# Performance work log

Hardware: AMD Instinct MI355X
Metric: run time of the kernel (lower is better)

## Reference

```python
import jax, jax.numpy as jnp
import numpy as np

N_STEPS = 8          # spatial_interval
SPATIAL_SCALE = 1.0  # spatial_scale


def setup_inputs() -> dict:
    key = jax.random.key(0)
    ks = jax.random.split(key, 6)
    B, N, D = 32, 1024, 256
    x = jax.random.normal(ks[0], (B, N, D), dtype=jnp.float32)
    adj_mx = jax.random.uniform(ks[1], (N, N), dtype=jnp.float32) / N  # row-scaled dense adjacency
    alpha_train = jnp.ones((N,), dtype=jnp.float32)          # alpha * ones(num_node), alpha=1.0
    w = jnp.eye(D, dtype=jnp.float32) + 0.01 * jax.random.normal(ks[2], (D, D), dtype=jnp.float32)
    d = jax.random.uniform(ks[3], (D,), dtype=jnp.float32)
    fc_in_w = jax.random.normal(ks[4], (D, D), dtype=jnp.float32) * (1.0 / np.sqrt(D))
    fc_in_b = jnp.zeros((D,), dtype=jnp.float32)
    return {"x": x, "adj_mx": adj_mx, "alpha_train": alpha_train, "w": w,
            "d": d, "fc_in_w": fc_in_w, "fc_in_b": fc_in_b, "vt": 0}


def reference(x, adj_mx, alpha_train, w, d, fc_in_w, fc_in_b, vt):
    # x: [B, N, D]. x0 is detached in torch (x.clone().detach()).
    x0 = jax.lax.stop_gradient(x)
    # fc_in (dropout is identity in eval mode)
    h = jnp.einsum('bnd,ed->bne', x, fc_in_w) + fc_in_b
    # constants of the diffusion ODE
    alph = jax.nn.sigmoid(alpha_train)[:, None]          # [N, 1]
    d_clamped = jnp.clip(d, 0.0, 1.0)
    w_eff = (w * d_clamped) @ w.T                        # [D, D]
    dt = jnp.float32(SPATIAL_SCALE / N_STEPS)

    def euler_step(h, _):
        ax = jnp.einsum('nm,bmd->bnd', adj_mx, h)        # graph diffusion
        f = alph * 0.5 * (ax - h) + h @ w_eff - h + x0
        return h + dt * f, None

    h, _ = jax.lax.scan(euler_step, h, None, length=N_STEPS)
    return h
```

## Files before the change

kernel.cpp:

```cpp
#include <hip/hip_runtime.h>
#include <hip/hip_bf16.h>
#include <stdint.h>

typedef __bf16 bf16;
typedef __bf16 bf16x8 __attribute__((ext_vector_type(8)));
typedef __bf16 bf16x4 __attribute__((ext_vector_type(4)));
typedef float f32x4 __attribute__((ext_vector_type(4)));
typedef unsigned short u16;

__device__ __forceinline__ void gload_lds16(const bf16* g, bf16* l) {
    __builtin_amdgcn_global_load_lds(
        (const __attribute__((address_space(1))) void*)g,
        (__attribute__((address_space(3))) void*)l, 16, 0, 0);
}

__device__ __forceinline__ void stChunk(const bf16* __restrict__ g, int ld,
                                        bf16* l, int c) {
    int row = c >> 3, slot = c & 7;
    gload_lds16(g + (size_t)row * ld + ((slot ^ (row & 7)) << 3), l + c * 8);
}

#define LDSW(buf, row, kc) \
    (*(const bf16x8*)&(buf)[(row) * 64 + ((((kc) ^ ((row) & 7))) << 3)])

__global__ void prep_alpha(const float* __restrict__ a, float* __restrict__ out) {
    int i = blockIdx.x * blockDim.x + threadIdx.x;
    if (i < 1024) out[i] = 0.5f / (1.0f + __expf(-a[i]));
}

__global__ void prep_adj(const float* __restrict__ adj, const float* __restrict__ ahs,
                         bf16* __restrict__ adjb) {
    int i = blockIdx.x * blockDim.x + threadIdx.x;
    int row = i >> 8;
    float s = ahs[row];
    float4 v = ((const float4*)adj)[i];
    bf16x4 o = {(bf16)(s * v.x), (bf16)(s * v.y), (bf16)(s * v.z), (bf16)(s * v.w)};
    ((bf16x4*)adjb)[i] = o;
}

__global__ void cast_f32_bf16x4(const float* __restrict__ src, bf16* __restrict__ dst,
                                int n4) {
    int i = blockIdx.x * blockDim.x + threadIdx.x;
    if (i < n4) {
        float4 v = ((const float4*)src)[i];
        bf16x4 o = {(bf16)v.x, (bf16)v.y, (bf16)v.z, (bf16)v.w};
        ((bf16x4*)dst)[i] = o;
    }
}

__global__ void prep_weff(const float* __restrict__ w, const float* __restrict__ dv,
                          bf16* __restrict__ weffT) {
    __shared__ float wk[256];
    __shared__ float dd[256];
    int k = blockIdx.x, j = threadIdx.x;
    dd[j] = fminf(fmaxf(dv[j], 0.0f), 1.0f);
    wk[j] = w[k * 256 + j];
    __syncthreads();
    float s = 0.0f;
#pragma unroll 8
    for (int c = 0; c < 256; ++c) s += wk[c] * dd[c] * w[j * 256 + c];
    weffT[j * 256 + k] = (bf16)s;
}

__global__ void prep_xT(const float* __restrict__ x, bf16* __restrict__ xT,
                        bf16* __restrict__ xb) {
    __shared__ bf16 tile[64][65];
    int b = blockIdx.z, n0 = blockIdx.x * 64, d0 = blockIdx.y * 64;
    int t = threadIdx.x;
    int i = t >> 4, j4 = (t & 15) * 4;
#pragma unroll
    for (int p = 0; p < 4; ++p) {
        int n = i + p * 16;
        size_t gi = (((size_t)b << 10) + n0 + n) * 256 + d0 + j4;
        float4 v = *(const float4*)&x[gi];
        bf16x4 o = {(bf16)v.x, (bf16)v.y, (bf16)v.z, (bf16)v.w};
        *(bf16x4*)&xb[gi] = o;
        tile[n][j4 + 0] = o[0]; tile[n][j4 + 1] = o[1];
        tile[n][j4 + 2] = o[2]; tile[n][j4 + 3] = o[3];
    }
    __syncthreads();
#pragma unroll
    for (int p = 0; p < 4; ++p) {
        int c = p * 256 + t;
        int d = c >> 4, nc = c & 15;
        bf16x4 o = {tile[nc * 4 + 0][d], tile[nc * 4 + 1][d],
                    tile[nc * 4 + 2][d], tile[nc * 4 + 3][d]};
        *(bf16x4*)&xT[(((size_t)(b * 256 + d0 + d)) << 10) + n0 + nc * 4] = o;
    }
}

__device__ __forceinline__ void stageA4(const bf16* __restrict__ g, int lda,
                                        bf16* l, int t) {
#pragma unroll
    for (int i = 0; i < 4; ++i) stChunk(g, lda, l, (i << 8) + t);
}
__device__ __forceinline__ void stageB2(const bf16* __restrict__ g, int ldb,
                                        bf16* l, int t) {
#pragma unroll
    for (int i = 0; i < 2; ++i) stChunk(g, ldb, l, (i << 8) + t);
}

__device__ __forceinline__ void mma_tile(const bf16* A, const bf16* B,
                                         f32x4 acc[2][4], int lane, int wv) {
    const int r0 = wv * 32 + (lane & 15);
    const int kq = lane >> 4;
    bf16x8 a[2][2], b[4][2];
#pragma unroll
    for (int mi = 0; mi < 2; ++mi) {
        int rA = r0 + mi * 16;
#pragma unroll
        for (int kk = 0; kk < 2; ++kk) a[mi][kk] = LDSW(A, rA, kk * 4 + kq);
    }
#pragma unroll
    for (int ni = 0; ni < 4; ++ni) {
        int rB = ni * 16 + (lane & 15);
#pragma unroll
        for (int kk = 0; kk < 2; ++kk) b[ni][kk] = LDSW(B, rB, kk * 4 + kq);
    }
#pragma unroll
    for (int kk = 0; kk < 2; ++kk)
#pragma unroll
        for (int mi = 0; mi < 2; ++mi)
#pragma unroll
            for (int ni = 0; ni < 4; ++ni)
                acc[mi][ni] = __builtin_amdgcn_mfma_f32_16x16x32_bf16(
                    a[mi][kk], b[ni][kk], acc[mi][ni], 0, 0, 0);
}

template <int NT, typename F>
__device__ __forceinline__ void run_pipeline(F tadr, bf16 (*As)[8192],
                                             bf16 (*Bs)[4096], f32x4 acc[2][4],
                                             int t, int lane, int wv) {
    {
        const bf16 *Ag, *Bg; int lda, ldb;
        tadr(0, Ag, lda, Bg, ldb);
        stageA4(Ag, lda, As[0], t);
        stageB2(Bg, ldb, Bs[0], t);
        if (NT > 1) {
            tadr(1, Ag, lda, Bg, ldb);
            stageA4(Ag, lda, As[1], t);
            stageB2(Bg, ldb, Bs[1], t);
        }
    }
    int cur = 0, pre = 2;
#pragma unroll 1
    for (int i = 0; i < NT; ++i) {
        if (i + 2 < NT) {
            const bf16 *Ag, *Bg; int lda, ldb;
            tadr(i + 2, Ag, lda, Bg, ldb);
            stageA4(Ag, lda, As[pre], t);
            stageB2(Bg, ldb, Bs[pre], t);
            asm volatile("s_waitcnt vmcnt(12)" ::: "memory");
        } else if (i + 1 < NT) {
            asm volatile("s_waitcnt vmcnt(6)" ::: "memory");
        } else {
            asm volatile("s_waitcnt vmcnt(0)" ::: "memory");
        }
        __builtin_amdgcn_s_barrier();
        __builtin_amdgcn_s_setprio(1);
        mma_tile(As[cur], Bs[cur], acc, lane, wv);
        __builtin_amdgcn_s_setprio(0);
        __builtin_amdgcn_s_barrier();
        cur = (cur == 2) ? 0 : cur + 1;
        pre = (pre == 2) ? 0 : pre + 1;
    }
}

__launch_bounds__(256, 2)
__global__ void gemm_fcin(const bf16* __restrict__ xb, const bf16* __restrict__ fcwb,
                          const float* __restrict__ fcb,
                          bf16* __restrict__ hb, bf16* __restrict__ hT,
                          bf16* __restrict__ hloT) {
    __shared__ __align__(16) bf16 As[3][8192];
    __shared__ __align__(16) bf16 Bs[3][4096];
    int t = threadIdx.x, lane = t & 63, wv = t >> 6;
    int row0 = blockIdx.y * 128;
    int col0 = blockIdx.x * 64;
    f32x4 acc[2][4] = {};
    const bf16* Ab = xb + (size_t)row0 * 256;
    const bf16* Bb = fcwb + (size_t)col0 * 256;
    auto tadr = [&](int i, const bf16*& Ag, int& lda, const bf16*& Bg, int& ldb) {
        Ag = Ab + i * 64; lda = 256;
        Bg = Bb + i * 64; ldb = 256;
    };
    run_pipeline<4>(tadr, As, Bs, acc, t, lane, wv);

    int rbase = row0 + wv * 32 + ((lane >> 4) << 2);
    int cbase = col0 + (lane & 15);
#pragma unroll
    for (int mi = 0; mi < 2; ++mi) {
        int rg = rbase + mi * 16;
#pragma unroll
        for (int ni = 0; ni < 4; ++ni) {
            int col = cbase + ni * 16;
            float bias = fcb[col];
            bf16x4 tv, lv;
#pragma unroll
            for (int r = 0; r < 4; ++r) {
                float v = acc[mi][ni][r] + bias;
                size_t idx = (size_t)(rg + r) * 256 + col;
                bf16 hi = (bf16)v;
                hb[idx] = hi;
                tv[r] = hi;
                lv[r] = (bf16)(v - (float)hi);
            }
            int b = rg >> 10, n = rg & 1023;
            size_t tb = (((size_t)(b * 256 + col)) << 10) + n;
            *(bf16x4*)&hT[tb] = tv;
            *(bf16x4*)&hloT[tb] = lv;
        }
    }
}

template <bool LAST>
__launch_bounds__(512, 1)
__global__ void gemm_step(const bf16* __restrict__ adjb, const bf16* __restrict__ hbp,
                          const bf16* __restrict__ hTp, const bf16* __restrict__ weffT,
                          const float* __restrict__ ahs, const bf16* __restrict__ xT,
                          bf16* __restrict__ hloT, bf16* __restrict__ hbn,
                          bf16* __restrict__ hTn, float* __restrict__ out) {
    __shared__ __align__(16) char smem[147456];
    bf16 (*As)[16384] = (bf16(*)[16384])smem;
    bf16 (*Bs)[8192]  = (bf16(*)[8192])(smem + 98304);
    int t = threadIdx.x, lane = t & 63, wv = t >> 6;
    int wm = wv >> 1, wn = wv & 1;
    int g = blockIdx.x;
    int xcd = g & 7, bidx = g >> 3;
    int b = (bidx & 3) * 8 + xcd;
    int tile = bidx >> 2;
    int n0 = (tile & 3) * 256;
    int d0 = (tile >> 2) * 128;
    f32x4 acc[4][4] = {};

    const bf16* A1 = adjb + (size_t)n0 * 1024;
    const bf16* B1 = hTp + ((size_t)(b * 256 + d0)) * 1024;
    const bf16* A2 = hbp + ((size_t)(b * 1024 + n0)) * 256;
    const bf16* B2 = weffT + (size_t)d0 * 256;
    auto tadr = [&](int i, const bf16*& Ag, int& la, const bf16*& Bg, int& lb) {
        if (i < 16) { Ag = A1 + i * 64; la = 1024; Bg = B1 + i * 64; lb = 1024; }
        else        { Ag = A2 + (i - 16) * 64; la = 256; Bg = B2 + (i - 16) * 64; lb = 256; }
    };
    const int NT = 20;
    {
        const bf16 *Ag, *Bg; int la, lb;
        tadr(0, Ag, la, Bg, lb);
#pragma unroll
        for (int k = 0; k < 4; ++k) stChunk(Ag, la, As[0], k * 512 + t);
#pragma unroll
        for (int k = 0; k < 2; ++k) stChunk(Bg, lb, Bs[0], k * 512 + t);
        tadr(1, Ag, la, Bg, lb);
#pragma unroll
        for (int k = 0; k < 4; ++k) stChunk(Ag, la, As[1], k * 512 + t);
#pragma unroll
        for (int k = 0; k < 2; ++k) stChunk(Bg, lb, Bs[1], k * 512 + t);
    }
    const int l15 = lane & 15, kq = lane >> 4;
    const int rA[4] = {wm * 64 + l15, wm * 64 + 16 + l15,
                       wm * 64 + 32 + l15, wm * 64 + 48 + l15};
    const int rB[4] = {wn * 64 + l15, wn * 64 + 16 + l15,
                       wn * 64 + 32 + l15, wn * 64 + 48 + l15};

    asm volatile("s_waitcnt vmcnt(6)" ::: "memory");
    __builtin_amdgcn_s_barrier();

    bf16x8 pa[4], pb[4];
#pragma unroll
    for (int j = 0; j < 4; ++j) pb[j] = LDSW(Bs[0], rB[j], kq);
#pragma unroll
    for (int j = 0; j < 4; ++j) pa[j] = LDSW(As[0], rA[j], kq);

    int cur = 0;
#pragma unroll 1
    for (int i = 0; i < NT; ++i) {
        const bf16* Ab = As[cur];
        const bf16* Bb = Bs[cur];
        int nxt = cur + 1; if (nxt == 3) nxt = 0;
        int pre = cur + 2; if (pre >= 3) pre -= 3;
        const bool st2 = (i + 2 < NT), st1 = (i + 1 < NT);
        const bf16 *Ag = nullptr, *Bg = nullptr; int la = 0, lb = 0;
        if (st2) tadr(i + 2, Ag, la, Bg, lb);

        bf16x8 qa[4], qb[4];
#pragma unroll
        for (int j = 0; j < 4; ++j) qb[j] = LDSW(Bb, rB[j], 4 + kq);
#pragma unroll
        for (int j = 0; j < 4; ++j) qa[j] = LDSW(Ab, rA[j], 4 + kq);
        if (st2) {
            stChunk(Ag, la, As[pre], t);        stChunk(Ag, la, As[pre], 512 + t);
            stChunk(Ag, la, As[pre], 1024 + t); stChunk(Ag, la, As[pre], 1536 + t);
        }
        __builtin_amdgcn_s_barrier();
        asm volatile("s_waitcnt lgkmcnt(8)" ::: "memory");
        __builtin_amdgcn_sched_barrier(0);
        __builtin_amdgcn_s_setprio(1);
#pragma unroll
        for (int mi = 0; mi < 4; ++mi)
#pragma unroll
            for (int ni = 0; ni < 4; ++ni)
                acc[mi][ni] = __builtin_amdgcn_mfma_f32_16x16x32_bf16(
                    pa[mi], pb[ni], acc[mi][ni], 0, 0, 0);
        __builtin_amdgcn_s_setprio(0);
        __builtin_amdgcn_s_barrier();

        if (st2) {
            stChunk(Bg, lb, Bs[pre], t); stChunk(Bg, lb, Bs[pre], 512 + t);
            asm volatile("s_waitcnt vmcnt(6)" ::: "memory");
        } else {
            asm volatile("s_waitcnt vmcnt(0)" ::: "memory");
        }
        __builtin_amdgcn_s_barrier();
        if (st1) {
            const bf16* An = As[nxt];
            const bf16* Bn = Bs[nxt];
#pragma unroll
            for (int j = 0; j < 4; ++j) pb[j] = LDSW(Bn, rB[j], kq);
#pragma unroll
            for (int j = 0; j < 4; ++j) pa[j] = LDSW(An, rA[j], kq);
            asm volatile("s_waitcnt lgkmcnt(8)" ::: "memory");
        } else {
            asm volatile("s_waitcnt lgkmcnt(0)" ::: "memory");
        }
        __builtin_amdgcn_sched_barrier(0);
        __builtin_amdgcn_s_setprio(1);
#pragma unroll
        for (int mi = 0; mi < 4; ++mi)
#pragma unroll
            for (int ni = 0; ni < 4; ++ni)
                acc[mi][ni] = __builtin_amdgcn_mfma_f32_16x16x32_bf16(
                    qa[mi], qb[ni], acc[mi][ni], 0, 0, 0);
        __builtin_amdgcn_s_setprio(0);
        __builtin_amdgcn_s_barrier();
        cur = nxt;
    }

    const float dt = 0.125f;
    const int lq = (lane >> 4) << 2;
    bf16* img = (bf16*)smem;
    const int PADN = 260;
#pragma unroll
    for (int mi = 0; mi < 4; ++mi) {
        int nl = wm * 64 + mi * 16 + lq;
        int ng = n0 + nl;
        f32x4 av = *(const f32x4*)&ahs[ng];
#pragma unroll
        for (int ni = 0; ni < 4; ++ni) {
            int cl = wn * 64 + ni * 16 + l15;
            int cg = d0 + cl;
            size_t tb = (((size_t)(b * 256 + cg)) << 10) + ng;
            bf16x4 hp = *(const bf16x4*)&hTp[tb];
            bf16x4 lp = *(const bf16x4*)&hloT[tb];
            bf16x4 xp = *(const bf16x4*)&xT[tb];
            bf16x4 nhi, nlo;
#pragma unroll
            for (int r = 0; r < 4; ++r) {
                float hold = (float)hp[r] + (float)lp[r];
                float f = acc[mi][ni][r] - (av[r] + 1.0f) * hold + (float)xp[r];
                float hv = hold + dt * f;
                if (LAST) {
                    out[(((size_t)b << 10) + ng + r) * 256 + cg] = hv;
                } else {
                    bf16 hi2 = (bf16)hv;
                    nhi[r] = hi2;
                    nlo[r] = (bf16)(hv - (float)hi2);
                }
            }
            if (!LAST) {
                *(bf16x4*)&hTn[tb] = nhi;
                *(bf16x4*)&hloT[tb] = nlo;
                int nsw = nl ^ (((cl >> 3) & 7) << 2);
                *(bf16x4*)&img[cl * PADN + nsw] = nhi;
            }
        }
    }
    if (!LAST) {
        asm volatile("s_waitcnt lgkmcnt(0)" ::: "memory");
        __builtin_amdgcn_s_barrier();
        const u16* imgu = (const u16*)img;
#pragma unroll
        for (int P = 0; P < 8; ++P) {
            int chunk = P * 512 + t;
            int node = chunk >> 4;
            int c8 = chunk & 15;
            u16 v[8];
#pragma unroll
            for (int k = 0; k < 8; ++k) {
                int col = c8 * 8 + k;
                v[k] = imgu[col * PADN + (node ^ (((col >> 3) & 7) << 2))];
            }
            uint4 pk;
            pk.x = v[0] | ((unsigned)v[1] << 16);
            pk.y = v[2] | ((unsigned)v[3] << 16);
            pk.z = v[4] | ((unsigned)v[5] << 16);
            pk.w = v[6] | ((unsigned)v[7] << 16);
            *(uint4*)&hbn[(((size_t)b << 10) + n0 + node) * 256 + d0 + c8 * 8] = pk;
        }
    }
}

extern "C" void kernel_launch(void* const* d_in, const int* in_sizes, int n_in,
                              void* d_out, int out_size, void* d_ws, size_t ws_size,
                              hipStream_t stream) {
    const float* x     = (const float*)d_in[0];
    const float* adj   = (const float*)d_in[1];
    const float* alpha = (const float*)d_in[2];
    const float* w     = (const float*)d_in[3];
    const float* dvec  = (const float*)d_in[4];
    const float* fcw   = (const float*)d_in[5];
    const float* fcb   = (const float*)d_in[6];
    float* out = (float*)d_out;

    const size_t HB = (size_t)32 * 1024 * 256 * 2;
    char* p = (char*)d_ws;
    bf16* hb0   = (bf16*)p; p += HB;
    bf16* hb1   = (bf16*)p; p += HB;
    bf16* hT0   = (bf16*)p; p += HB;
    bf16* hT1   = (bf16*)p; p += HB;
    bf16* xb    = (bf16*)p; p += HB;
    bf16* hloT  = (bf16*)p; p += HB;
    bf16* xT    = (bf16*)p; p += HB;
    bf16* adjb  = (bf16*)p; p += (size_t)1024 * 1024 * 2;
    bf16* fcwb  = (bf16*)p; p += 256 * 256 * 2;
    bf16* weffT = (bf16*)p; p += 256 * 256 * 2;
    float* ahs  = (float*)p; p += 1024 * 4;

    prep_alpha<<<4, 256, 0, stream>>>(alpha, ahs);
    prep_adj<<<1024, 256, 0, stream>>>(adj, ahs, adjb);
    prep_weff<<<256, 256, 0, stream>>>(w, dvec, weffT);
    prep_xT<<<dim3(16, 4, 32), 256, 0, stream>>>(x, xT, xb);
    cast_f32_bf16x4<<<64, 256, 0, stream>>>(fcw, fcwb, 16384);

    gemm_fcin<<<dim3(4, 256), 256, 0, stream>>>(xb, fcwb, fcb, hb0, hT0, hloT);

    bf16* hb[2] = {hb0, hb1};
    bf16* hT[2] = {hT0, hT1};
    int cur = 0;
    for (int s = 0; s < 8; ++s) {
        if (s < 7)
            gemm_step<false><<<256, 512, 0, stream>>>(
                adjb, hb[cur], hT[cur], weffT, ahs, xT, hloT,
                hb[cur ^ 1], hT[cur ^ 1], out);
        else
            gemm_step<true><<<256, 512, 0, stream>>>(
                adjb, hb[cur], hT[cur], weffT, ahs, xT, hloT,
                hb[cur ^ 1], hT[cur ^ 1], out);
        cur ^= 1;
    }
}
```

Measured before the change: 397.3 us.

## Shrink gemm_step tiles to 128x128 with 256 threads and double buffering

Restructures the per-step fused GEMM from 256x128 tiles with 512 threads, a triple-buffered LDS ring and register-prefetched fragments into 128x128 tiles with 256 threads, two LDS buffers and a simpler load-then-compute loop. The grid grows from 256 to 512 blocks and LDS drops to 64KB, so two blocks can share a CU for better occupancy and latency hiding. It also removes the s_setprio hints in the fc_in GEMM. The cost is less reuse per block (adjacency and h tiles are re-read more often) and the loss of the hand-tuned overlap between LDS fragment loads and MFMAs.

Result: faster. 378.3 us (-4.8%).

```diff
diff --git a/kernel.cpp b/kernel.cpp
--- a/kernel.cpp
+++ b/kernel.cpp
@@ -14,10 +14,13 @@
         (__attribute__((address_space(3))) void*)l, 16, 0, 0);
 }
 
-__device__ __forceinline__ void stChunk(const bf16* __restrict__ g, int ld,
-                                        bf16* l, int c) {
-    int row = c >> 3, slot = c & 7;
-    gload_lds16(g + (size_t)row * ld + ((slot ^ (row & 7)) << 3), l + c * 8);
+template <int LD>
+__device__ __forceinline__ void stage(const bf16* __restrict__ g, bf16* l, int t) {
+    int sw = ((t & 7) ^ ((t >> 3) & 7)) << 3;
+    size_t base = (size_t)(t >> 3) * LD + sw;
+#pragma unroll
+    for (int k = 0; k < 4; ++k)
+        gload_lds16(g + base + (size_t)(k * 32) * LD, l + t * 8 + k * 2048);
 }
 
 #define LDSW(buf, row, kc) \
@@ -89,6 +92,11 @@
     }
 }
 
+__device__ __forceinline__ void stChunk(const bf16* __restrict__ g, int ld,
+                                        bf16* l, int c) {
+    int row = c >> 3, slot = c & 7;
+    gload_lds16(g + (size_t)row * ld + ((slot ^ (row & 7)) << 3), l + c * 8);
+}
 __device__ __forceinline__ void stageA4(const bf16* __restrict__ g, int lda,
                                         bf16* l, int t) {
 #pragma unroll
@@ -157,9 +165,7 @@
             asm volatile("s_waitcnt vmcnt(0)" ::: "memory");
         }
         __builtin_amdgcn_s_barrier();
-        __builtin_amdgcn_s_setprio(1);
         mma_tile(As[cur], Bs[cur], acc, lane, wv);
-        __builtin_amdgcn_s_setprio(0);
         __builtin_amdgcn_s_barrier();
         cur = (cur == 2) ? 0 : cur + 1;
         pre = (pre == 2) ? 0 : pre + 1;
@@ -213,130 +219,80 @@
 }
 
 template <bool LAST>
-__launch_bounds__(512, 1)
+__launch_bounds__(256, 2)
 __global__ void gemm_step(const bf16* __restrict__ adjb, const bf16* __restrict__ hbp,
                           const bf16* __restrict__ hTp, const bf16* __restrict__ weffT,
                           const float* __restrict__ ahs, const bf16* __restrict__ xT,
                           bf16* __restrict__ hloT, bf16* __restrict__ hbn,
                           bf16* __restrict__ hTn, float* __restrict__ out) {
-    __shared__ __align__(16) char smem[147456];
-    bf16 (*As)[16384] = (bf16(*)[16384])smem;
-    bf16 (*Bs)[8192]  = (bf16(*)[8192])(smem + 98304);
+    __shared__ __align__(16) char smem[65536];
+    bf16 (*As)[8192] = (bf16(*)[8192])smem;
+    bf16 (*Bs)[8192] = (bf16(*)[8192])(smem + 32768);
     int t = threadIdx.x, lane = t & 63, wv = t >> 6;
     int wm = wv >> 1, wn = wv & 1;
     int g = blockIdx.x;
-    int xcd = g & 7, bidx = g >> 3;
-    int b = (bidx & 3) * 8 + xcd;
-    int tile = bidx >> 2;
-    int n0 = (tile & 3) * 256;
-    int d0 = (tile >> 2) * 128;
+    int xcd = g & 7, rest = g >> 3;
+    int b = (rest & 3) * 8 + xcd;
+    int tile = rest >> 2;
+    int n0 = (tile & 7) * 128;
+    int d0 = (tile >> 3) * 128;
     f32x4 acc[4][4] = {};
 
     const bf16* A1 = adjb + (size_t)n0 * 1024;
     const bf16* B1 = hTp + ((size_t)(b * 256 + d0)) * 1024;
     const bf16* A2 = hbp + ((size_t)(b * 1024 + n0)) * 256;
     const bf16* B2 = weffT + (size_t)d0 * 256;
-    auto tadr = [&](int i, const bf16*& Ag, int& la, const bf16*& Bg, int& lb) {
-        if (i < 16) { Ag = A1 + i * 64; la = 1024; Bg = B1 + i * 64; lb = 1024; }
-        else        { Ag = A2 + (i - 16) * 64; la = 256; Bg = B2 + (i - 16) * 64; lb = 256; }
-    };
-    const int NT = 20;
-    {
-        const bf16 *Ag, *Bg; int la, lb;
-        tadr(0, Ag, la, Bg, lb);
-#pragma unroll
-        for (int k = 0; k < 4; ++k) stChunk(Ag, la, As[0], k * 512 + t);
-#pragma unroll
-        for (int k = 0; k < 2; ++k) stChunk(Bg, lb, Bs[0], k * 512 + t);
-        tadr(1, Ag, la, Bg, lb);
-#pragma unroll
-        for (int k = 0; k < 4; ++k) stChunk(Ag, la, As[1], k * 512 + t);
-#pragma unroll
-        for (int k = 0; k < 2; ++k) stChunk(Bg, lb, Bs[1], k * 512 + t);
-    }
+
     const int l15 = lane & 15, kq = lane >> 4;
-    const int rA[4] = {wm * 64 + l15, wm * 64 + 16 + l15,
-                       wm * 64 + 32 + l15, wm * 64 + 48 + l15};
-    const int rB[4] = {wn * 64 + l15, wn * 64 + 16 + l15,
-                       wn * 64 + 32 + l15, wn * 64 + 48 + l15};
-
-    asm volatile("s_waitcnt vmcnt(6)" ::: "memory");
-    __builtin_amdgcn_s_barrier();
-
-    bf16x8 pa[4], pb[4];
-#pragma unroll
-    for (int j = 0; j < 4; ++j) pb[j] = LDSW(Bs[0], rB[j], kq);
-#pragma unroll
-    for (int j = 0; j < 4; ++j) pa[j] = LDSW(As[0], rA[j], kq);
-
-    int cur = 0;
+    int rA[4], rB[4];
+#pragma unroll
+    for (int j = 0; j < 4; ++j) {
+        rA[j] = wm * 64 + j * 16 + l15;
+        rB[j] = wn * 64 + j * 16 + l15;
+    }
+
+    stage<1024>(A1, As[0], t);
+    stage<1024>(B1, Bs[0], t);
+
 #pragma unroll 1
-    for (int i = 0; i < NT; ++i) {
-        const bf16* Ab = As[cur];
-        const bf16* Bb = Bs[cur];
-        int nxt = cur + 1; if (nxt == 3) nxt = 0;
-        int pre = cur + 2; if (pre >= 3) pre -= 3;
-        const bool st2 = (i + 2 < NT), st1 = (i + 1 < NT);
-        const bf16 *Ag = nullptr, *Bg = nullptr; int la = 0, lb = 0;
-        if (st2) tadr(i + 2, Ag, la, Bg, lb);
-
-        bf16x8 qa[4], qb[4];
-#pragma unroll
-        for (int j = 0; j < 4; ++j) qb[j] = LDSW(Bb, rB[j], 4 + kq);
-#pragma unroll
-        for (int j = 0; j < 4; ++j) qa[j] = LDSW(Ab, rA[j], 4 + kq);
-        if (st2) {
-            stChunk(Ag, la, As[pre], t);        stChunk(Ag, la, As[pre], 512 + t);
-            stChunk(Ag, la, As[pre], 1024 + t); stChunk(Ag, la, As[pre], 1536 + t);
-        }
-        __builtin_amdgcn_s_barrier();
-        asm volatile("s_waitcnt lgkmcnt(8)" ::: "memory");
-        __builtin_amdgcn_sched_barrier(0);
-        __builtin_amdgcn_s_setprio(1);
-#pragma unroll
-        for (int mi = 0; mi < 4; ++mi)
-#pragma unroll
-            for (int ni = 0; ni < 4; ++ni)
-                acc[mi][ni] = __builtin_amdgcn_mfma_f32_16x16x32_bf16(
-                    pa[mi], pb[ni], acc[mi][ni], 0, 0, 0);
-        __builtin_amdgcn_s_setprio(0);
-        __builtin_amdgcn_s_barrier();
-
-        if (st2) {
-            stChunk(Bg, lb, Bs[pre], t); stChunk(Bg, lb, Bs[pre], 512 + t);
-            asm volatile("s_waitcnt vmcnt(6)" ::: "memory");
+    for (int i = 0; i < 20; ++i) {
+        if (i + 1 < 20) {
+            if (i + 1 < 16) {
+                stage<1024>(A1 + (i + 1) * 64, As[(i + 1) & 1], t);
+                stage<1024>(B1 + (i + 1) * 64, Bs[(i + 1) & 1], t);
+            } else {
+                stage<256>(A2 + (i - 15) * 64, As[(i + 1) & 1], t);
+                stage<256>(B2 + (i - 15) * 64, Bs[(i + 1) & 1], t);
+            }
+            asm volatile("s_waitcnt vmcnt(8)" ::: "memory");
         } else {
             asm volatile("s_waitcnt vmcnt(0)" ::: "memory");
         }
         __builtin_amdgcn_s_barrier();
-        if (st1) {
-            const bf16* An = As[nxt];
-            const bf16* Bn = Bs[nxt];
-#pragma unroll
-            for (int j = 0; j < 4; ++j) pb[j] = LDSW(Bn, rB[j], kq);
-#pragma unroll
-            for (int j = 0; j < 4; ++j) pa[j] = LDSW(An, rA[j], kq);
-            asm volatile("s_waitcnt lgkmcnt(8)" ::: "memory");
-        } else {
-            asm volatile("s_waitcnt lgkmcnt(0)" ::: "memory");
-        }
-        __builtin_amdgcn_sched_barrier(0);
-        __builtin_amdgcn_s_setprio(1);
-#pragma unroll
-        for (int mi = 0; mi < 4; ++mi)
-#pragma unroll
-            for (int ni = 0; ni < 4; ++ni)
-                acc[mi][ni] = __builtin_amdgcn_mfma_f32_16x16x32_bf16(
-                    qa[mi], qb[ni], acc[mi][ni], 0, 0, 0);
-        __builtin_amdgcn_s_setprio(0);
+        const bf16* A = As[i & 1];
+        const bf16* B = Bs[i & 1];
+#pragma unroll
+        for (int kk = 0; kk < 2; ++kk) {
+            int kc = kk * 4 + kq;
+            bf16x8 a[4], bfr[4];
+#pragma unroll
+            for (int j = 0; j < 4; ++j) bfr[j] = LDSW(B, rB[j], kc);
+#pragma unroll
+            for (int j = 0; j < 4; ++j) a[j] = LDSW(A, rA[j], kc);
+#pragma unroll
+            for (int mi = 0; mi < 4; ++mi)
+#pragma unroll
+                for (int ni = 0; ni < 4; ++ni)
+                    acc[mi][ni] = __builtin_amdgcn_mfma_f32_16x16x32_bf16(
+                        a[mi], bfr[ni], acc[mi][ni], 0, 0, 0);
+        }
         __builtin_amdgcn_s_barrier();
-        cur = nxt;
     }
 
     const float dt = 0.125f;
     const int lq = (lane >> 4) << 2;
     bf16* img = (bf16*)smem;
-    const int PADN = 260;
+    const int PADN = 132;
 #pragma unroll
     for (int mi = 0; mi < 4; ++mi) {
         int nl = wm * 64 + mi * 16 + lq;
@@ -378,7 +334,7 @@
         const u16* imgu = (const u16*)img;
 #pragma unroll
         for (int P = 0; P < 8; ++P) {
-            int chunk = P * 512 + t;
+            int chunk = P * 256 + t;
             int node = chunk >> 4;
             int c8 = chunk & 15;
             u16 v[8];
@@ -436,11 +392,11 @@
     int cur = 0;
     for (int s = 0; s < 8; ++s) {
         if (s < 7)
-            gemm_step<false><<<256, 512, 0, stream>>>(
+            gemm_step<false><<<512, 256, 0, stream>>>(
                 adjb, hb[cur], hT[cur], weffT, ahs, xT, hloT,
                 hb[cur ^ 1], hT[cur ^ 1], out);
         else
-            gemm_step<true><<<256, 512, 0, stream>>>(
+            gemm_step<true><<<512, 256, 0, stream>>>(
                 adjb, hb[cur], hT[cur], weffT, ahs, xT, hloT,
                 hb[cur ^ 1], hT[cur ^ 1], out);
         cur ^= 1;
```
